# Performance work log

Measured on AMD Instinct MI355X. Metric: run time of the kernel, lower is better.

Reference implementation:

```python
import jax, jax.numpy as jnp
import numpy as np

B, V, T, CIN, WEMB, H, NW = 32, 500, 24, 2, 4, 64, 8
C0 = CIN + WEMB  # 6 channels entering first layer


def _stglstm(x, supports, Wg, bg, Wo, bo, out_len=None, final_layer=False):
    # x: (B, C, V, T); supports: (S, V, V)
    Bb, C, Vv, Tt = x.shape
    T_steps = out_len if out_len is not None else Tt
    if final_layer:
        xs = jnp.broadcast_to(x[:, :, :, -1][None], (T_steps, Bb, C, Vv))
    else:
        xs = jnp.moveaxis(x, 3, 0)  # (T, B, C, V)

    def step(carry, xt):
        hx, cx = carry
        comb = xt + hx  # (B, C, V)
        feats = [comb]
        for s in range(supports.shape[0]):  # fixed small support_len loop
            x1 = jnp.einsum('bcv,vw->bcw', comb, supports[s])
            x2 = jnp.einsum('bcv,vw->bcw', x1, supports[s])
            feats += [x1, x2]  # order-2 diffusion
        g = jnp.concatenate(feats, axis=1)  # (B, 7C, V)
        gates = jnp.einsum('bgv,og->bov', g, Wg) + bg[None, :, None]  # (B, 4C, V)
        i, f, cg, o = jnp.split(gates, 4, axis=1)
        cy = jax.nn.sigmoid(f) * cx + jax.nn.sigmoid(i) * cg  # cellgate is linear (no tanh), as in source
        hy = jax.nn.sigmoid(o) * jnp.tanh(cy)
        return (hy, cy), hy

    h0 = jnp.zeros((Bb, C, Vv), x.dtype)
    _, hs = jax.lax.scan(step, (h0, h0), xs)  # hs: (T, B, C, V)
    hs = jnp.moveaxis(hs, 0, 3)  # (B, C, V, T)
    return jnp.einsum('bcvt,oc->bovt', hs, Wo) + bo[None, :, None, None]


def _se(x, Wa, Wb):
    y = x.mean(axis=(2, 3))  # (B, C) global avg pool
    y = jax.nn.sigmoid(jax.nn.relu(y @ Wa.T) @ Wb.T)
    return x * y[:, :, None, None]


def setup_inputs():
    key = jax.random.key(0)
    ks = jax.random.split(key, 24)

    def n(k, shape, s=0.05):
        return jax.random.normal(k, shape, jnp.float32) * s

    A = jax.random.uniform(ks[0], (3, V, V), jnp.float32)
    A = A / A.sum(-1, keepdims=True)  # row-stochastic random-walk matrices
    return {
        'x': n(ks[1], (B, CIN, V, T), 1.0),
        'supports': A,
        'w_type': jax.random.randint(ks[2], (B, V, T), 0, NW, dtype=jnp.int32),
        'Wemb': n(ks[3], (NW, WEMB)),
        'Wg0': n(ks[4], (4 * C0, 7 * C0)), 'bg0': jnp.zeros((4 * C0,), jnp.float32),
        'Wo0': n(ks[5], (H, C0)), 'bo0': jnp.zeros((H,), jnp.float32),
        'Ws0a': n(ks[6], (H // 16, H)), 'Ws0b': n(ks[7], (H, H // 16)),
        'Wg1': n(ks[8], (4 * H, 7 * H)), 'bg1': jnp.zeros((4 * H,), jnp.float32),
        'Wo1': n(ks[9], (H, H)), 'bo1': jnp.zeros((H,), jnp.float32),
        'Ws1a': n(ks[10], (H // 16, H)), 'Ws1b': n(ks[11], (H, H // 16)),
        'Wg2': n(ks[12], (4 * H, 7 * H)), 'bg2': jnp.zeros((4 * H,), jnp.float32),
        'Wo2': n(ks[13], (H, H)), 'bo2': jnp.zeros((H,), jnp.float32),
        'Wg3': n(ks[14], (4 * H, 7 * H)), 'bg3': jnp.zeros((4 * H,), jnp.float32),
        'Wo3': n(ks[15], (2, H)), 'bo3': jnp.zeros((2,), jnp.float32),
    }


def reference(x, supports, w_type, Wemb, Wg0, bg0, Wo0, bo0, Ws0a, Ws0b,
              Wg1, bg1, Wo1, bo1, Ws1a, Ws1b, Wg2, bg2, Wo2, bo2,
              Wg3, bg3, Wo3, bo3):
    w_vec = Wemb[w_type]  # (B, V, T, wemb)
    w_vec = jnp.transpose(w_vec, (0, 3, 1, 2))  # (B, wemb, V, T)
    h = jnp.concatenate([x, w_vec], axis=1)  # (B, CIN+wemb, V, T)
    h = _stglstm(h, supports, Wg0, bg0, Wo0, bo0)
    h = _se(h, Ws0a, Ws0b)
    h = _stglstm(h, supports, Wg1, bg1, Wo1, bo1)
    h = _se(h, Ws1a, Ws1b)
    h = _stglstm(h, supports, Wg2, bg2, Wo2, bo2)
    out = _stglstm(h, supports, Wg3, bg3, Wo3, bo3, out_len=T, final_layer=True)
    return out  # (B, 2, V, out_len)
```

## Files before the change

### kernel.cpp

```cpp
#include <hip/hip_runtime.h>
#include <math.h>

#define NV 500
#define NB 32
#define NT 24
#define NH 64

typedef _Float16 f16;
typedef _Float16 f16x8 __attribute__((ext_vector_type(8)));
typedef _Float16 f16x4 __attribute__((ext_vector_type(4)));
typedef float    f32x4 __attribute__((ext_vector_type(4)));

__device__ __forceinline__ float sigm(float x){ return 1.f/(1.f+expf(-x)); }

__global__ void k_a2(const float* __restrict__ A, float* __restrict__ A2)
{
    int idx = blockIdx.x*256 + threadIdx.x;
    if (idx >= 3*500*500) return;
    int wv = idx % 500; int rest = idx/500; int r = rest % 500; int s = rest/500;
    const float* Ar = A + ((size_t)s*500 + r)*500;
    const float* Ac = A + (size_t)s*500*500 + wv;
    float a = 0.f;
    for (int u = 0; u < 500; u++) a += Ar[u]*Ac[(size_t)u*500];
    A2[idx] = a;
}

__global__ void k_acat(const float* __restrict__ A, const float* __restrict__ A2,
                       f16* __restrict__ AcatT)
{
    int idx = blockIdx.x*256 + threadIdx.x;
    if (idx >= 3072*512) return;
    int k = idx & 511;
    int n = idx >> 9;
    int j = n >> 9, wv = n & 511;
    float val = 0.f;
    if (k < 500 && wv < 500) {
        int s = j >> 1;
        const float* M = (j & 1) ? A2 : A;
        val = M[((size_t)s*500 + k)*500 + wv];
    }
    AcatT[idx] = (f16)val;
}

__global__ void k_f2h(const float* __restrict__ src, f16* __restrict__ dst, int n)
{
    int idx = blockIdx.x*256 + threadIdx.x;
    if (idx < n) dst[idx] = (f16)src[idx];
}

__global__ __launch_bounds__(256)
void k_diff(const f16* __restrict__ Acv, const f16* __restrict__ Bt,
            f16* __restrict__ fout, int Mtot, int C, int G)
{
    __shared__ f16 lA[128*32];
    __shared__ f16 lB[128*32];
    const int tid = threadIdx.x;
    const int n0 = blockIdx.x*128, m0 = blockIdx.y*128;
    const int r0 = tid>>2, c0 = tid&3;
    const int swz0 = r0*32 + ((c0 ^ ((r0>>1)&3))<<3);
    const int swz1 = swz0 + 64*32;
    int mA0 = m0 + r0;      if (mA0 > Mtot-1) mA0 = Mtot-1;
    int mA1 = m0 + r0 + 64; if (mA1 > Mtot-1) mA1 = Mtot-1;
    const f16* gA0 = Acv + (size_t)mA0*512 + c0*8;
    const f16* gA1 = Acv + (size_t)mA1*512 + c0*8;
    const f16* gB0 = Bt + (size_t)(n0+r0)*512 + c0*8;
    const f16* gB1 = Bt + (size_t)(n0+r0+64)*512 + c0*8;

    const int w = tid>>6, lane = tid&63;
    const int wr = (w>>1)<<6, wc = (w&1)<<6;
    const int fm = lane&15, fk = lane>>4;
    const int fch = (fk ^ ((fm>>1)&3))<<3;

    f32x4 acc[4][4];
    #pragma unroll
    for (int i=0;i<4;i++)
        #pragma unroll
        for (int j=0;j<4;j++) acc[i][j] = (f32x4){0.f,0.f,0.f,0.f};

    f32x4 ra0 = *(const f32x4*)gA0, ra1 = *(const f32x4*)gA1;
    f32x4 rb0 = *(const f32x4*)gB0, rb1 = *(const f32x4*)gB1;

    for (int ks = 0; ks < 16; ks++) {
        __syncthreads();
        *(f32x4*)(lA + swz0) = ra0;  *(f32x4*)(lA + swz1) = ra1;
        *(f32x4*)(lB + swz0) = rb0;  *(f32x4*)(lB + swz1) = rb1;
        if (ks < 15) {
            int o = (ks+1)*32;
            ra0 = *(const f32x4*)(gA0 + o); ra1 = *(const f32x4*)(gA1 + o);
            rb0 = *(const f32x4*)(gB0 + o); rb1 = *(const f32x4*)(gB1 + o);
        }
        __syncthreads();
        f16x8 af[4], bf[4];
        #pragma unroll
        for (int i=0;i<4;i++) af[i] = *(const f16x8*)(lA + (wr + i*16 + fm)*32 + fch);
        #pragma unroll
        for (int j=0;j<4;j++) bf[j] = *(const f16x8*)(lB + (wc + j*16 + fm)*32 + fch);
        #pragma unroll
        for (int i=0;i<4;i++)
            #pragma unroll
            for (int j=0;j<4;j++)
                acc[i][j] = __builtin_amdgcn_mfma_f32_16x16x32_f16(af[i], bf[j], acc[i][j], 0, 0, 0);
    }

    #pragma unroll
    for (int j=0;j<4;j++) {
        int col = n0 + wc + j*16 + fm;
        int jb = col >> 9, wv = col & 511;
        if (wv >= 500) continue;
        #pragma unroll
        for (int i=0;i<4;i++) {
            int mb = m0 + wr + i*16 + fk*4;
            if (C == 64) {
                if (mb >= Mtot) continue;
                int b = mb >> 6, c = mb & 63;
                f16x4 h4;
                h4[0]=(f16)acc[i][j][0]; h4[1]=(f16)acc[i][j][1];
                h4[2]=(f16)acc[i][j][2]; h4[3]=(f16)acc[i][j][3];
                *(f16x4*)(fout + ((size_t)b*512 + wv)*G + C + jb*C + c) = h4;
            } else {
                #pragma unroll
                for (int r=0;r<4;r++) {
                    int m = mb + r;
                    if (m < Mtot) {
                        int b = m / C, c = m - b*C;
                        fout[((size_t)b*512 + wv)*G + C + jb*C + c] = (f16)acc[i][j][r];
                    }
                }
            }
        }
    }
}

__global__ __launch_bounds__(256)
void k_gateslstm(const f16* __restrict__ fT, const f16* __restrict__ Wg,
                 const float* __restrict__ bg, float* __restrict__ cst,
                 const f16* __restrict__ Xn, f16* __restrict__ hsave,
                 const float* __restrict__ Wo3, const float* __restrict__ bo3,
                 float* __restrict__ out, int t,
                 f16* __restrict__ fTout, f16* __restrict__ ccv,
                 int first, int writecomb)
{
    __shared__ f16 lA[64*32];
    __shared__ f16 lB[256*32];
    __shared__ float ExF[4*64*65];
    __shared__ float bgS[256];
    __shared__ f16 combS[64*68];
    const int tid = threadIdx.x;
    const int m0 = blockIdx.x*64, b = blockIdx.y;
    const f16* Ab = fT + (size_t)b*512*448;
    bgS[tid] = bg[tid];

    const int r0 = tid>>2, c0 = tid&3;
    const int swz = r0*32 + ((c0 ^ ((r0>>1)&3))<<3);
    const f16* gA = Ab + (size_t)(m0+r0)*448 + c0*8;
    const f16* gB = Wg + (size_t)r0*448 + c0*8;

    const int w = tid>>6, lane = tid&63;
    const int wc = w<<6;
    const int fm = lane&15, fk = lane>>4;
    const int fch = (fk ^ ((fm>>1)&3))<<3;

    f32x4 acc[4][4];
    #pragma unroll
    for (int i=0;i<4;i++)
        #pragma unroll
        for (int j=0;j<4;j++) acc[i][j] = (f32x4){0.f,0.f,0.f,0.f};

    f32x4 ra  = *(const f32x4*)gA;
    f32x4 rb0 = *(const f32x4*)gB;
    f32x4 rb1 = *(const f32x4*)(gB + (size_t)64*448);
    f32x4 rb2 = *(const f32x4*)(gB + (size_t)128*448);
    f32x4 rb3 = *(const f32x4*)(gB + (size_t)192*448);

    for (int ks = 0; ks < 14; ks++) {
        __syncthreads();
        *(f32x4*)(lA + swz) = ra;
        *(f32x4*)(lB + swz)          = rb0;
        *(f32x4*)(lB + 64*32 + swz)  = rb1;
        *(f32x4*)(lB + 128*32 + swz) = rb2;
        *(f32x4*)(lB + 192*32 + swz) = rb3;
        if (ks < 13) {
            int o = (ks+1)*32;
            ra  = *(const f32x4*)(gA + o);
            rb0 = *(const f32x4*)(gB + o);
            rb1 = *(const f32x4*)(gB + (size_t)64*448 + o);
            rb2 = *(const f32x4*)(gB + (size_t)128*448 + o);
            rb3 = *(const f32x4*)(gB + (size_t)192*448 + o);
        }
        __syncthreads();
        f16x8 af[4], bf[4];
        #pragma unroll
        for (int i=0;i<4;i++) af[i] = *(const f16x8*)(lA + (i*16 + fm)*32 + fch);
        #pragma unroll
        for (int j=0;j<4;j++) bf[j] = *(const f16x8*)(lB + (wc + j*16 + fm)*32 + fch);
        #pragma unroll
        for (int i=0;i<4;i++)
            #pragma unroll
            for (int j=0;j<4;j++)
                acc[i][j] = __builtin_amdgcn_mfma_f32_16x16x32_f16(af[i], bf[j], acc[i][j], 0, 0, 0);
    }

    __syncthreads();
    #pragma unroll
    for (int i=0;i<4;i++)
        #pragma unroll
        for (int j=0;j<4;j++)
            #pragma unroll
            for (int r=0;r<4;r++)
                ExF[((w<<6) + i*16 + (fk<<2) + r)*65 + (j<<4) + fm] = acc[i][j][r];
    __syncthreads();

    const int vl = tid>>2, p = tid&3;
    const int v = m0 + vl;
    const size_t row = (size_t)b*512 + v;
    float hy[16];
    float* cp = cst + row*64 + (p<<4);
    #pragma unroll
    for (int k4=0;k4<4;k4++) {
        f32x4 cx4 = first ? (f32x4){0.f,0.f,0.f,0.f} : *(const f32x4*)(cp + k4*4);
        f32x4 cy4;
        #pragma unroll
        for (int e=0;e<4;e++) {
            int c = (p<<4) + k4*4 + e;
            float gi = ExF[(         vl)*65 + c] + bgS[c];
            float gf = ExF[( 64 +    vl)*65 + c] + bgS[64+c];
            float gc = ExF[(128 +    vl)*65 + c] + bgS[128+c];
            float go = ExF[(192 +    vl)*65 + c] + bgS[192+c];
            float cy = sigm(gf)*cx4[e] + sigm(gi)*gc;
            cy4[e] = cy;
            hy[k4*4+e] = sigm(go)*tanhf(cy);
        }
        *(f32x4*)(cp + k4*4) = cy4;
    }

    if (hsave) {
        alignas(16) f16 tmp[16];
        #pragma unroll
        for (int k=0;k<16;k++) tmp[k] = (f16)hy[k];
        f16* hp = hsave + row*64 + (p<<4);
        *(f32x4*)hp = *(f32x4*)tmp;
        *(f32x4*)(hp+8) = *(f32x4*)(tmp+8);
    }

    if (out) {
        float r0s = 0.f, r1s = 0.f;
        #pragma unroll
        for (int k=0;k<16;k++){ r0s += Wo3[(p<<4)+k]*hy[k]; r1s += Wo3[64+(p<<4)+k]*hy[k]; }
        r0s += __shfl_xor(r0s, 1, 64); r0s += __shfl_xor(r0s, 2, 64);
        r1s += __shfl_xor(r1s, 1, 64); r1s += __shfl_xor(r1s, 2, 64);
        if (p == 0 && v < 500) {
            out[((size_t)(b*2+0)*500 + v)*24 + t] = r0s + bo3[0];
            out[((size_t)(b*2+1)*500 + v)*24 + t] = r1s + bo3[1];
        }
    }

    if (writecomb) {
        alignas(16) f16 c16[16];
        if (v < 500) {
            const f16* xp = Xn + row*64 + (p<<4);
            alignas(16) f16 xv[16];
            *(f32x4*)xv = *(const f32x4*)xp;
            *(f32x4*)(xv+8) = *(const f32x4*)(xp+8);
            #pragma unroll
            for (int k=0;k<16;k++) c16[k] = (f16)((float)xv[k] + hy[k]);
        } else {
            #pragma unroll
            for (int k=0;k<16;k++) c16[k] = (f16)0.f;
        }
        f16* fp = fTout + row*448 + (p<<4);
        *(f32x4*)fp = *(f32x4*)c16;
        *(f32x4*)(fp+8) = *(f32x4*)(c16+8);
        #pragma unroll
        for (int k=0;k<16;k++) combS[vl*68 + (p<<4) + k] = c16[k];
        __syncthreads();
        const int c = tid>>2, jj = tid&3;
        alignas(16) f16 tmp[16];
        #pragma unroll
        for (int k=0;k<16;k++) tmp[k] = combS[(jj*16+k)*68 + c];
        f16* dst = ccv + ((size_t)b*64 + c)*512 + m0 + jj*16;
        *(f32x4*)dst = *(f32x4*)tmp;
        *(f32x4*)(dst+8) = *(f32x4*)(tmp+8);
    }
}

__global__ __launch_bounds__(256)
void k_seed(const f16* __restrict__ X0, f16* __restrict__ fT, f16* __restrict__ ccv)
{
    __shared__ f16 combS[64*68];
    const int b = blockIdx.y, v0 = blockIdx.x*64;
    const int tid = threadIdx.x, vl = tid>>2, p = tid&3;
    const int v = v0 + vl;
    const size_t row = (size_t)b*512 + v;
    alignas(16) f16 c16[16];
    if (v < 500) {
        const f16* xp = X0 + row*64 + p*16;
        *(f32x4*)c16 = *(const f32x4*)xp;
        *(f32x4*)(c16+8) = *(const f32x4*)(xp+8);
    } else {
        #pragma unroll
        for (int k=0;k<16;k++) c16[k] = (f16)0.f;
    }
    f16* fp = fT + row*448 + p*16;
    *(f32x4*)fp = *(f32x4*)c16;
    *(f32x4*)(fp+8) = *(f32x4*)(c16+8);
    #pragma unroll
    for (int k=0;k<16;k++) combS[vl*68 + p*16 + k] = c16[k];
    __syncthreads();
    const int c = tid>>2, j = tid&3;
    alignas(16) f16 tmp[16];
    #pragma unroll
    for (int k=0;k<16;k++) tmp[k] = combS[(j*16+k)*68 + c];
    f16* dst = ccv + ((size_t)b*64 + c)*512 + v0 + j*16;
    *(f32x4*)dst = *(f32x4*)tmp;
    *(f32x4*)(dst+8) = *(f32x4*)(tmp+8);
}

__global__ __launch_bounds__(256)
void k_xprojm(const f16* __restrict__ src, const f16* __restrict__ WoF,
              const float* __restrict__ bo, const float* __restrict__ se,
              f16* __restrict__ X)
{
    __shared__ f16 lA[128*64];
    __shared__ f16 lB[64*64];
    const int tid = threadIdx.x;
    const size_t m0 = (size_t)blockIdx.x*128;
    const int r0 = tid>>2, c0 = tid&3;
    const int swz = r0*32 + ((c0 ^ ((r0>>1)&3))<<3);
    const f16* gA0 = src + (m0 + r0)*64 + c0*8;
    const f16* gA1 = gA0 + 64*64;
    const f16* gB  = WoF + r0*64 + c0*8;

    *(f32x4*)(lA + swz)               = *(const f32x4*)gA0;
    *(f32x4*)(lA + 2048 + swz)        = *(const f32x4*)gA1;
    *(f32x4*)(lA + 4096 + swz)        = *(const f32x4*)(gA0 + 32);
    *(f32x4*)(lA + 6144 + swz)        = *(const f32x4*)(gA1 + 32);
    *(f32x4*)(lB + swz)               = *(const f32x4*)gB;
    *(f32x4*)(lB + 2048 + swz)        = *(const f32x4*)(gB + 32);
    __syncthreads();

    const int w = tid>>6, lane = tid&63;
    const int wr = w<<5;
    const int fm = lane&15, fk = lane>>4;
    const int fch = (fk ^ ((fm>>1)&3))<<3;

    f32x4 acc[2][4];
    #pragma unroll
    for (int i=0;i<2;i++)
        #pragma unroll
        for (int j=0;j<4;j++) acc[i][j] = (f32x4){0.f,0.f,0.f,0.f};

    #pragma unroll
    for (int ks=0; ks<2; ks++) {
        f16x8 af[2], bf[4];
        #pragma unroll
        for (int i=0;i<2;i++) af[i] = *(const f16x8*)(lA + ks*4096 + (wr + i*16 + fm)*32 + fch);
        #pragma unroll
        for (int j=0;j<4;j++) bf[j] = *(const f16x8*)(lB + ks*2048 + (j*16 + fm)*32 + fch);
        #pragma unroll
        for (int i=0;i<2;i++)
            #pragma unroll
            for (int j=0;j<4;j++)
                acc[i][j] = __builtin_amdgcn_mfma_f32_16x16x32_f16(af[i], bf[j], acc[i][j], 0, 0, 0);
    }
    __syncthreads();

    const int bb = (int)((m0 >> 9) & 31);
    #pragma unroll
    for (int j=0;j<4;j++) {
        const int c = (j<<4) + fm;
        const float bias = bo[c];
        const float sf = se ? se[bb*64 + c] : 1.f;
        #pragma unroll
        for (int i=0;i<2;i++) {
            const int rbase = wr + i*16 + (fk<<2);
            #pragma unroll
            for (int r=0;r<4;r++)
                lA[(rbase + r)*64 + c] = (f16)(sf*(acc[i][j][r] + bias));
        }
    }
    __syncthreads();
    #pragma unroll
    for (int pass=0; pass<4; pass++) {
        int chunk = pass*256 + tid;
        int row = chunk>>3, off = (chunk&7)<<3;
        *(f32x4*)(X + (m0 + row)*64 + off) = *(const f32x4*)(lA + row*64 + off);
    }
}

__global__ void k_xproj1(const float* __restrict__ src, const float* __restrict__ Wo,
                         const float* __restrict__ bo, const float* __restrict__ se,
                         f16* __restrict__ X, int total)
{
    int id = blockIdx.x*256 + threadIdx.x;
    if (id >= total) return;
    int c = id & 63;
    size_t row = (size_t)(id >> 6);
    int b = (int)((row >> 9) & 31);
    const float* sp = src + row*6;
    float a = bo[c];
    #pragma unroll
    for (int j=0;j<6;j++) a += Wo[c*6+j]*sp[j];
    X[id] = (f16)(se[b*64+c]*a);
}

__global__ void k_xe(const float* __restrict__ x, const int* __restrict__ wt,
                     const float* __restrict__ Wemb, float* __restrict__ XE)
{
    int id = blockIdx.x*256 + threadIdx.x;
    if (id >= NT*NB*512) return;
    int v = id & 511; int r = id >> 9; int b = r & 31; int t = r >> 5;
    float vals[6] = {0.f,0.f,0.f,0.f,0.f,0.f};
    if (v < 500) {
        vals[0] = x[((size_t)(b*2+0)*500 + v)*24 + t];
        vals[1] = x[((size_t)(b*2+1)*500 + v)*24 + t];
        int wty = wt[((size_t)b*500 + v)*24 + t];
        vals[2] = Wemb[wty*4+0]; vals[3] = Wemb[wty*4+1];
        vals[4] = Wemb[wty*4+2]; vals[5] = Wemb[wty*4+3];
    }
    float* xe = XE + (size_t)id*6;
    #pragma unroll
    for (int c = 0; c < 6; c++) xe[c] = vals[c];
}

__global__ void k_seed0(const float* __restrict__ XE, f16* __restrict__ f0T,
                        f16* __restrict__ ccv0)
{
    int id = blockIdx.x*256 + threadIdx.x;
    if (id >= NB*512) return;
    int v = id & 511, b = id >> 9;
    const float* xe = XE + (size_t)id*6;
    #pragma unroll
    for (int c = 0; c < 6; c++) {
        f16 h = (v < 500) ? (f16)xe[c] : (f16)0.f;
        f0T[(size_t)id*42 + c] = h;
        ccv0[((size_t)b*6 + c)*512 + v] = h;
    }
}

__global__ __launch_bounds__(256)
void k_glstm0(f16* f0T, const float* __restrict__ Wg0,
              const float* __restrict__ bg0, float* __restrict__ cst0,
              float* __restrict__ hs0T, const float* __restrict__ XE,
              f16* __restrict__ ccv0, int t)
{
    __shared__ float WgS[24*42];
    __shared__ float bgS[24];
    int tid = threadIdx.x;
    for (int i = tid; i < 24*42; i += 256) WgS[i] = Wg0[i];
    if (tid < 24) bgS[tid] = bg0[tid];
    __syncthreads();
    int id = blockIdx.x*256 + tid;
    if (id >= NB*500) return;
    int b = id / 500, v = id - b*500;
    const f16* fp = f0T + ((size_t)b*512 + v)*42;
    float fv[42];
    #pragma unroll
    for (int g = 0; g < 42; g++) fv[g] = (float)fp[g];
    float gates[24];
    #pragma unroll
    for (int o = 0; o < 24; o++) {
        float a = bgS[o];
        #pragma unroll
        for (int g = 0; g < 42; g++) a += WgS[o*42+g]*fv[g];
        gates[o] = a;
    }
    size_t hrow = (((size_t)t*NB + b)*512 + v)*6;
    const float* xe = XE + (((size_t)(t+1)*NB + b)*512 + v)*6;
    #pragma unroll
    for (int c = 0; c < 6; c++) {
        size_t ci = ((size_t)b*500 + v)*6 + c;
        float cx = t ? cst0[ci] : 0.f;
        float cy = sigm(gates[6+c])*cx + sigm(gates[c])*gates[12+c];
        cst0[ci] = cy;
        float h = sigm(gates[18+c])*tanhf(cy);
        hs0T[hrow + c] = h;
        if (t < 23) {
            float cmb = xe[c] + h;
            f0T[((size_t)b*512 + v)*42 + c] = (f16)cmb;
            ccv0[((size_t)b*6 + c)*512 + v] = (f16)cmb;
        }
    }
}

__global__ void k_mean0(const float* __restrict__ hs0T, float* __restrict__ mean0)
{
    int b = blockIdx.x;
    float acc[6] = {0,0,0,0,0,0};
    for (int i = threadIdx.x; i < 24*500; i += 256) {
        int tt = i/500, v = i - tt*500;
        const float* p = hs0T + (((size_t)tt*NB + b)*512 + v)*6;
        #pragma unroll
        for (int c=0;c<6;c++) acc[c] += p[c];
    }
    __shared__ float red[256];
    for (int c=0;c<6;c++) {
        red[threadIdx.x] = acc[c]; __syncthreads();
        for (int s=128;s>0;s>>=1) { if (threadIdx.x<s) red[threadIdx.x]+=red[threadIdx.x+s]; __syncthreads(); }
        if (threadIdx.x==0) mean0[b*6+c] = red[0]/12000.f;
        __syncthreads();
    }
}

__global__ void k_mean1(const f16* __restrict__ hs1T, float* __restrict__ mean1)
{
    int cg = blockIdx.x, b = blockIdx.y;
    float acc[8] = {0,0,0,0,0,0,0,0};
    for (int i = threadIdx.x; i < 24*500; i += 256) {
        int tt = i/500, v = i - tt*500;
        const f16* p = hs1T + (((size_t)tt*NB + b)*512 + v)*64 + cg*8;
        #pragma unroll
        for (int c=0;c<8;c++) acc[c] += (float)p[c];
    }
    __shared__ float red[256];
    for (int c=0;c<8;c++) {
        red[threadIdx.x] = acc[c]; __syncthreads();
        for (int s=128;s>0;s>>=1) { if (threadIdx.x<s) red[threadIdx.x]+=red[threadIdx.x+s]; __syncthreads(); }
        if (threadIdx.x==0) mean1[b*64 + cg*8 + c] = red[0]/12000.f;
        __syncthreads();
    }
}

__global__ void k_se(const float* __restrict__ meanhs, const float* __restrict__ Wo,
                     const float* __restrict__ bo, int Cin,
                     const float* __restrict__ Wa, const float* __restrict__ Wb,
                     float* __restrict__ se)
{
    int b = blockIdx.x; int c = threadIdx.x;
    __shared__ float y[64]; __shared__ float a[4];
    float acc = bo[c];
    for (int j = 0; j < Cin; j++) acc += Wo[(size_t)c*Cin + j] * meanhs[b*Cin + j];
    y[c] = acc;
    __syncthreads();
    if (c < 4) {
        float s = 0.f;
        for (int j = 0; j < 64; j++) s += Wa[c*64 + j] * y[j];
        a[c] = fmaxf(s, 0.f);
    }
    __syncthreads();
    float s = 0.f;
    #pragma unroll
    for (int j = 0; j < 4; j++) s += Wb[c*4 + j] * a[j];
    se[b*64 + c] = 1.f/(1.f + expf(-s));
}

extern "C" void kernel_launch(void* const* d_in, const int* in_sizes, int n_in,
                              void* d_out, int out_size, void* d_ws, size_t ws_size,
                              hipStream_t stream)
{
    const float* x    = (const float*)d_in[0];
    const float* sup  = (const float*)d_in[1];
    const int*   wt   = (const int*)  d_in[2];
    const float* Wemb = (const float*)d_in[3];
    const float* Wg0  = (const float*)d_in[4];
    const float* bg0  = (const float*)d_in[5];
    const float* Wo0  = (const float*)d_in[6];
    const float* bo0  = (const float*)d_in[7];
    const float* Wa0  = (const float*)d_in[8];
    const float* Wb0  = (const float*)d_in[9];
    const float* Wg1  = (const float*)d_in[10];
    const float* bg1  = (const float*)d_in[11];
    const float* Wo1  = (const float*)d_in[12];
    const float* bo1  = (const float*)d_in[13];
    const float* Wa1  = (const float*)d_in[14];
    const float* Wb1  = (const float*)d_in[15];
    const float* Wg2  = (const float*)d_in[16];
    const float* bg2  = (const float*)d_in[17];
    const float* Wo2  = (const float*)d_in[18];
    const float* bo2  = (const float*)d_in[19];
    const float* Wg3  = (const float*)d_in[20];
    const float* bg3  = (const float*)d_in[21];
    const float* Wo3  = (const float*)d_in[22];
    const float* bo3  = (const float*)d_in[23];
    float* out = (float*)d_out;
    (void)in_sizes; (void)n_in; (void)out_size; (void)ws_size;

    char* ws = (char*)d_ws;
    size_t off = 0;
    f16*   AcatT  = (f16*)(ws + off);   off += (size_t)3072*512*2;
    float* A2     = (float*)(ws + off); off += (size_t)3*500*500*4;
    f16*   WgF1   = (f16*)(ws + off);   off += (size_t)256*448*2;
    f16*   WgF2   = (f16*)(ws + off);   off += (size_t)256*448*2;
    f16*   WgF3   = (f16*)(ws + off);   off += (size_t)256*448*2;
    f16*   WoF1   = (f16*)(ws + off);   off += (size_t)64*64*2;
    f16*   WoF2   = (f16*)(ws + off);   off += (size_t)64*64*2;
    f16*   comb_cv= (f16*)(ws + off);   off += (size_t)2048*512*2;
    f16*   ccv0   = (f16*)(ws + off);   off += (size_t)192*512*2;
    f16*   featsT = (f16*)(ws + off);   off += (size_t)NB*512*448*2;
    f16*   f0T    = (f16*)(ws + off);   off += (size_t)NB*512*42*2;
    float* XE     = (float*)(ws + off); off += (size_t)NT*NB*512*6*4;
    float* hs0T   = (float*)(ws + off); off += (size_t)NT*NB*512*6*4;
    f16*   hs1T   = (f16*)(ws + off);   off += (size_t)NT*NB*512*64*2;
    f16*   hT     = (f16*)(ws + off);   off += (size_t)NB*512*64*2;
    float* cstT   = (float*)(ws + off); off += (size_t)NB*512*64*4;
    float* cst0   = (float*)(ws + off); off += (size_t)NB*500*6*4;
    f16*   Xbuf   = (f16*)(ws + off);   off += (size_t)NT*NB*512*64*2;
    f16*   X3     = (f16*)(ws + off);   off += (size_t)NB*512*64*2;
    float* mean0  = (float*)(ws + off); off += 8192;
    float* se0    = (float*)(ws + off); off += 8192;
    float* mean1  = (float*)(ws + off); off += 8192;
    float* se1    = (float*)(ws + off); off += 8192;

    const size_t sliceH = (size_t)NB*512*64;

    k_a2  <<<(3*500*500 + 255)/256, 256, 0, stream>>>(sup, A2);
    k_acat<<<(3072*512 + 255)/256, 256, 0, stream>>>(sup, A2, AcatT);
    k_f2h <<<(256*448 + 255)/256, 256, 0, stream>>>(Wg1, WgF1, 256*448);
    k_f2h <<<(256*448 + 255)/256, 256, 0, stream>>>(Wg2, WgF2, 256*448);
    k_f2h <<<(256*448 + 255)/256, 256, 0, stream>>>(Wg3, WgF3, 256*448);
    k_f2h <<<16, 256, 0, stream>>>(Wo1, WoF1, 64*64);
    k_f2h <<<16, 256, 0, stream>>>(Wo2, WoF2, 64*64);
    k_xe  <<<(NT*NB*512)/256, 256, 0, stream>>>(x, wt, Wemb, XE);

    k_seed0<<<(NB*512)/256, 256, 0, stream>>>(XE, f0T, ccv0);
    for (int t = 0; t < NT; t++) {
        k_diff  <<<dim3(24, 2), 256, 0, stream>>>(ccv0, AcatT, f0T, 192, 6, 42);
        k_glstm0<<<(NB*500 + 255)/256, 256, 0, stream>>>(f0T, Wg0, bg0, cst0, hs0T, XE, ccv0, t);
    }
    k_mean0<<<NB, 256, 0, stream>>>(hs0T, mean0);
    k_se   <<<NB, 64, 0, stream>>>(mean0, Wo0, bo0, 6, Wa0, Wb0, se0);

    k_xproj1<<<(NT*NB*512*64)/256, 256, 0, stream>>>(hs0T, Wo0, bo0, se0, Xbuf, NT*NB*512*64);
    k_seed <<<dim3(8, NB), 256, 0, stream>>>(Xbuf, featsT, comb_cv);
    for (int t = 0; t < NT; t++) {
        k_diff <<<dim3(24, 16), 256, 0, stream>>>(comb_cv, AcatT, featsT, 2048, 64, 448);
        k_gateslstm<<<dim3(8, NB), 256, 0, stream>>>(featsT, WgF1, bg1, cstT,
                 (t < 23) ? Xbuf + (size_t)(t+1)*sliceH : (const f16*)nullptr,
                 hs1T + (size_t)t*sliceH, nullptr, nullptr, nullptr, t,
                 featsT, comb_cv, t == 0, t < 23);
    }
    k_mean1<<<dim3(8, NB), 256, 0, stream>>>(hs1T, mean1);
    k_se   <<<NB, 64, 0, stream>>>(mean1, Wo1, bo1, 64, Wa1, Wb1, se1);

    k_xprojm<<<(NT*NB*512)/128, 256, 0, stream>>>(hs1T, WoF1, bo1, se1, Xbuf);
    k_seed <<<dim3(8, NB), 256, 0, stream>>>(Xbuf, featsT, comb_cv);
    for (int t = 0; t < NT; t++) {
        k_diff <<<dim3(24, 16), 256, 0, stream>>>(comb_cv, AcatT, featsT, 2048, 64, 448);
        k_gateslstm<<<dim3(8, NB), 256, 0, stream>>>(featsT, WgF2, bg2, cstT,
                 (t < 23) ? Xbuf + (size_t)(t+1)*sliceH : (const f16*)nullptr,
                 (t == 23) ? hT : (f16*)nullptr, nullptr, nullptr, nullptr, t,
                 featsT, comb_cv, t == 0, t < 23);
    }

    k_xprojm<<<(NB*512)/128, 256, 0, stream>>>(hT, WoF2, bo2, nullptr, X3);
    k_seed <<<dim3(8, NB), 256, 0, stream>>>(X3, featsT, comb_cv);
    for (int t = 0; t < NT; t++) {
        k_diff <<<dim3(24, 16), 256, 0, stream>>>(comb_cv, AcatT, featsT, 2048, 64, 448);
        k_gateslstm<<<dim3(8, NB), 256, 0, stream>>>(featsT, WgF3, bg3, cstT,
                 X3, nullptr, Wo3, bo3, out, t,
                 featsT, comb_cv, t == 0, t < 23);
    }
}
```

Measured before the change: 4.593 ms.

## Split gates GEMM from LSTM update and compute A² with MFMA GEMM

```diff
diff --git a/kernel.cpp b/kernel.cpp
--- a/kernel.cpp
+++ b/kernel.cpp
@@ -13,33 +13,95 @@
 
 __device__ __forceinline__ float sigm(float x){ return 1.f/(1.f+expf(-x)); }
 
-__global__ void k_a2(const float* __restrict__ A, float* __restrict__ A2)
-{
-    int idx = blockIdx.x*256 + threadIdx.x;
-    if (idx >= 3*500*500) return;
-    int wv = idx % 500; int rest = idx/500; int r = rest % 500; int s = rest/500;
-    const float* Ar = A + ((size_t)s*500 + r)*500;
-    const float* Ac = A + (size_t)s*500*500 + wv;
-    float a = 0.f;
-    for (int u = 0; u < 500; u++) a += Ar[u]*Ac[(size_t)u*500];
-    A2[idx] = a;
-}
-
-__global__ void k_acat(const float* __restrict__ A, const float* __restrict__ A2,
-                       f16* __restrict__ AcatT)
-{
-    int idx = blockIdx.x*256 + threadIdx.x;
-    if (idx >= 3072*512) return;
-    int k = idx & 511;
-    int n = idx >> 9;
-    int j = n >> 9, wv = n & 511;
-    float val = 0.f;
-    if (k < 500 && wv < 500) {
-        int s = j >> 1;
-        const float* M = (j & 1) ? A2 : A;
-        val = M[((size_t)s*500 + k)*500 + wv];
-    }
-    AcatT[idx] = (f16)val;
+__global__ __launch_bounds__(256)
+void k_prep_a(const float* __restrict__ A, f16* __restrict__ AcatT, f16* __restrict__ A16)
+{
+    __shared__ float t[64][65];
+    const int s = blockIdx.z;
+    const int v0 = blockIdx.y*64, w0 = blockIdx.x*64;
+    const float* As = A + (size_t)s*500*500;
+    const int tid = threadIdx.x;
+    for (int e = tid; e < 64*64; e += 256) {
+        int r = e>>6, c = e&63;
+        int v = v0+r, w = w0+c;
+        float val = (v < 500 && w < 500) ? As[(size_t)v*500 + w] : 0.f;
+        t[r][c] = val;
+        A16[((size_t)s*512 + v)*512 + w] = (f16)val;
+    }
+    __syncthreads();
+    for (int e = tid; e < 64*64; e += 256) {
+        int wr = e>>6, vc = e&63;
+        AcatT[((size_t)(2*s)*512 + w0+wr)*512 + v0+vc] = (f16)t[vc][wr];
+    }
+}
+
+__global__ __launch_bounds__(256)
+void k_a2m(f16* __restrict__ AcatT, const f16* __restrict__ A16)
+{
+    __shared__ f16 lA[128*32];
+    __shared__ f16 lB[128*32];
+    const int tid = threadIdx.x;
+    const int s = blockIdx.z;
+    const int n0 = blockIdx.x*128, m0 = blockIdx.y*128;
+    const f16* AT = AcatT + (size_t)(2*s)*512*512;
+    const f16* Y  = A16 + (size_t)s*512*512;
+    f16* D = AcatT + (size_t)(2*s+1)*512*512;
+
+    const int r0 = tid>>2, c0 = tid&3;
+    const int swz0 = r0*32 + ((c0 ^ ((r0>>1)&3))<<3);
+    const int swz1 = swz0 + 64*32;
+    const f16* gA0 = AT + (size_t)(m0+r0)*512 + c0*8;
+    const f16* gA1 = AT + (size_t)(m0+r0+64)*512 + c0*8;
+    const f16* gB0 = Y + (size_t)(n0+r0)*512 + c0*8;
+    const f16* gB1 = Y + (size_t)(n0+r0+64)*512 + c0*8;
+
+    const int w = tid>>6, lane = tid&63;
+    const int wr = (w>>1)<<6, wc = (w&1)<<6;
+    const int fm = lane&15, fk = lane>>4;
+    const int fch = (fk ^ ((fm>>1)&3))<<3;
+
+    f32x4 acc[4][4];
+    #pragma unroll
+    for (int i=0;i<4;i++)
+        #pragma unroll
+        for (int j=0;j<4;j++) acc[i][j] = (f32x4){0.f,0.f,0.f,0.f};
+
+    f32x4 ra0 = *(const f32x4*)gA0, ra1 = *(const f32x4*)gA1;
+    f32x4 rb0 = *(const f32x4*)gB0, rb1 = *(const f32x4*)gB1;
+
+    for (int ks = 0; ks < 16; ks++) {
+        __syncthreads();
+        *(f32x4*)(lA + swz0) = ra0;  *(f32x4*)(lA + swz1) = ra1;
+        *(f32x4*)(lB + swz0) = rb0;  *(f32x4*)(lB + swz1) = rb1;
+        if (ks < 15) {
+            int o = (ks+1)*32;
+            ra0 = *(const f32x4*)(gA0 + o); ra1 = *(const f32x4*)(gA1 + o);
+            rb0 = *(const f32x4*)(gB0 + o); rb1 = *(const f32x4*)(gB1 + o);
+        }
+        __syncthreads();
+        f16x8 af[4], bf[4];
+        #pragma unroll
+        for (int i=0;i<4;i++) af[i] = *(const f16x8*)(lA + (wr + i*16 + fm)*32 + fch);
+        #pragma unroll
+        for (int j=0;j<4;j++) bf[j] = *(const f16x8*)(lB + (wc + j*16 + fm)*32 + fch);
+        #pragma unroll
+        for (int i=0;i<4;i++)
+            #pragma unroll
+            for (int j=0;j<4;j++)
+                acc[i][j] = __builtin_amdgcn_mfma_f32_16x16x32_f16(af[i], bf[j], acc[i][j], 0, 0, 0);
+    }
+
+    #pragma unroll
+    for (int j=0;j<4;j++) {
+        int col = n0 + wc + j*16 + fm;
+        #pragma unroll
+        for (int i=0;i<4;i++) {
+            int mb = m0 + wr + i*16 + fk*4;
+            #pragma unroll
+            for (int r=0;r<4;r++)
+                D[(size_t)(mb+r)*512 + col] = (f16)acc[i][j][r];
+        }
+    }
 }
 
 __global__ void k_f2h(const float* __restrict__ src, f16* __restrict__ dst, int n)
@@ -132,31 +194,24 @@
 }
 
 __global__ __launch_bounds__(256)
-void k_gateslstm(const f16* __restrict__ fT, const f16* __restrict__ Wg,
-                 const float* __restrict__ bg, float* __restrict__ cst,
-                 const f16* __restrict__ Xn, f16* __restrict__ hsave,
-                 const float* __restrict__ Wo3, const float* __restrict__ bo3,
-                 float* __restrict__ out, int t,
-                 f16* __restrict__ fTout, f16* __restrict__ ccv,
-                 int first, int writecomb)
-{
-    __shared__ f16 lA[64*32];
-    __shared__ f16 lB[256*32];
-    __shared__ float ExF[4*64*65];
-    __shared__ float bgS[256];
-    __shared__ f16 combS[64*68];
+void k_gates(const f16* __restrict__ fT, const f16* __restrict__ Wg,
+             const float* __restrict__ bg, f16* __restrict__ gT)
+{
+    __shared__ f16 lA[128*32];
+    __shared__ f16 lB[128*32];
     const int tid = threadIdx.x;
-    const int m0 = blockIdx.x*64, b = blockIdx.y;
+    const int n0 = blockIdx.x*128, m0 = blockIdx.y*128, b = blockIdx.z;
     const f16* Ab = fT + (size_t)b*512*448;
-    bgS[tid] = bg[tid];
-
     const int r0 = tid>>2, c0 = tid&3;
-    const int swz = r0*32 + ((c0 ^ ((r0>>1)&3))<<3);
-    const f16* gA = Ab + (size_t)(m0+r0)*448 + c0*8;
-    const f16* gB = Wg + (size_t)r0*448 + c0*8;
+    const int swz0 = r0*32 + ((c0 ^ ((r0>>1)&3))<<3);
+    const int swz1 = swz0 + 64*32;
+    const f16* gA0 = Ab + (size_t)(m0+r0)*448 + c0*8;
+    const f16* gA1 = Ab + (size_t)(m0+r0+64)*448 + c0*8;
+    const f16* gB0 = Wg + (size_t)(n0+r0)*448 + c0*8;
+    const f16* gB1 = Wg + (size_t)(n0+r0+64)*448 + c0*8;
 
     const int w = tid>>6, lane = tid&63;
-    const int wc = w<<6;
+    const int wr = (w>>1)<<6, wc = (w&1)<<6;
     const int fm = lane&15, fk = lane>>4;
     const int fch = (fk ^ ((fm>>1)&3))<<3;
 
@@ -166,31 +221,22 @@
         #pragma unroll
         for (int j=0;j<4;j++) acc[i][j] = (f32x4){0.f,0.f,0.f,0.f};
 
-    f32x4 ra  = *(const f32x4*)gA;
-    f32x4 rb0 = *(const f32x4*)gB;
-    f32x4 rb1 = *(const f32x4*)(gB + (size_t)64*448);
-    f32x4 rb2 = *(const f32x4*)(gB + (size_t)128*448);
-    f32x4 rb3 = *(const f32x4*)(gB + (size_t)192*448);
+    f32x4 ra0 = *(const f32x4*)gA0, ra1 = *(const f32x4*)gA1;
+    f32x4 rb0 = *(const f32x4*)gB0, rb1 = *(const f32x4*)gB1;
 
     for (int ks = 0; ks < 14; ks++) {
         __syncthreads();
-        *(f32x4*)(lA + swz) = ra;
-        *(f32x4*)(lB + swz)          = rb0;
-        *(f32x4*)(lB + 64*32 + swz)  = rb1;
-        *(f32x4*)(lB + 128*32 + swz) = rb2;
-        *(f32x4*)(lB + 192*32 + swz) = rb3;
+        *(f32x4*)(lA + swz0) = ra0;  *(f32x4*)(lA + swz1) = ra1;
+        *(f32x4*)(lB + swz0) = rb0;  *(f32x4*)(lB + swz1) = rb1;
         if (ks < 13) {
             int o = (ks+1)*32;
-            ra  = *(const f32x4*)(gA + o);
-            rb0 = *(const f32x4*)(gB + o);
-            rb1 = *(const f32x4*)(gB + (size_t)64*448 + o);
-            rb2 = *(const f32x4*)(gB + (size_t)128*448 + o);
-            rb3 = *(const f32x4*)(gB + (size_t)192*448 + o);
+            ra0 = *(const f32x4*)(gA0 + o); ra1 = *(const f32x4*)(gA1 + o);
+            rb0 = *(const f32x4*)(gB0 + o); rb1 = *(const f32x4*)(gB1 + o);
         }
         __syncthreads();
         f16x8 af[4], bf[4];
         #pragma unroll
-        for (int i=0;i<4;i++) af[i] = *(const f16x8*)(lA + (i*16 + fm)*32 + fch);
+        for (int i=0;i<4;i++) af[i] = *(const f16x8*)(lA + (wr + i*16 + fm)*32 + fch);
         #pragma unroll
         for (int j=0;j<4;j++) bf[j] = *(const f16x8*)(lB + (wc + j*16 + fm)*32 + fch);
         #pragma unroll
@@ -200,35 +246,58 @@
                 acc[i][j] = __builtin_amdgcn_mfma_f32_16x16x32_f16(af[i], bf[j], acc[i][j], 0, 0, 0);
     }
 
-    __syncthreads();
-    #pragma unroll
-    for (int i=0;i<4;i++)
-        #pragma unroll
-        for (int j=0;j<4;j++)
-            #pragma unroll
-            for (int r=0;r<4;r++)
-                ExF[((w<<6) + i*16 + (fk<<2) + r)*65 + (j<<4) + fm] = acc[i][j][r];
-    __syncthreads();
-
-    const int vl = tid>>2, p = tid&3;
-    const int v = m0 + vl;
+    #pragma unroll
+    for (int j=0;j<4;j++) {
+        int o = n0 + wc + j*16 + fm;
+        float bias = bg[o];
+        #pragma unroll
+        for (int i=0;i<4;i++) {
+            int vb = m0 + wr + i*16 + fk*4;
+            #pragma unroll
+            for (int r=0;r<4;r++) {
+                int v = vb + r;
+                if (v < 500)
+                    gT[((size_t)b*512 + v)*256 + o] = (f16)(acc[i][j][r] + bias);
+            }
+        }
+    }
+}
+
+__global__ __launch_bounds__(256)
+void k_lstmcomb(const f16* __restrict__ gT, float* __restrict__ cst,
+                const f16* __restrict__ Xn, f16* __restrict__ hsave,
+                const float* __restrict__ Wo3, const float* __restrict__ bo3,
+                float* __restrict__ out, int t,
+                f16* __restrict__ fT, f16* __restrict__ ccv,
+                int first, int writecomb)
+{
+    __shared__ f16 combS[64*68];
+    const int b = blockIdx.y, v0 = blockIdx.x*64;
+    const int tid = threadIdx.x, vl = tid>>2, p = tid&3;
+    const int v = v0 + vl;
     const size_t row = (size_t)b*512 + v;
+    const f16* g = gT + row*256 + (p<<4);
+    alignas(16) f16 gq[4][16];
+    #pragma unroll
+    for (int q = 0; q < 4; q++) {
+        *(f32x4*)&gq[q][0] = *(const f32x4*)(g + q*64);
+        *(f32x4*)&gq[q][8] = *(const f32x4*)(g + q*64 + 8);
+    }
+
+    float* cp = cst + row*64 + (p<<4);
     float hy[16];
-    float* cp = cst + row*64 + (p<<4);
-    #pragma unroll
-    for (int k4=0;k4<4;k4++) {
+    #pragma unroll
+    for (int k4 = 0; k4 < 4; k4++) {
         f32x4 cx4 = first ? (f32x4){0.f,0.f,0.f,0.f} : *(const f32x4*)(cp + k4*4);
         f32x4 cy4;
         #pragma unroll
-        for (int e=0;e<4;e++) {
-            int c = (p<<4) + k4*4 + e;
-            float gi = ExF[(         vl)*65 + c] + bgS[c];
-            float gf = ExF[( 64 +    vl)*65 + c] + bgS[64+c];
-            float gc = ExF[(128 +    vl)*65 + c] + bgS[128+c];
-            float go = ExF[(192 +    vl)*65 + c] + bgS[192+c];
+        for (int e = 0; e < 4; e++) {
+            int kk = k4*4+e;
+            float gi = (float)gq[0][kk], gf = (float)gq[1][kk];
+            float gc = (float)gq[2][kk], go = (float)gq[3][kk];
             float cy = sigm(gf)*cx4[e] + sigm(gi)*gc;
             cy4[e] = cy;
-            hy[k4*4+e] = sigm(go)*tanhf(cy);
+            hy[kk] = sigm(go)*tanhf(cy);
         }
         *(f32x4*)(cp + k4*4) = cy4;
     }
@@ -243,14 +312,14 @@
     }
 
     if (out) {
-        float r0s = 0.f, r1s = 0.f;
-        #pragma unroll
-        for (int k=0;k<16;k++){ r0s += Wo3[(p<<4)+k]*hy[k]; r1s += Wo3[64+(p<<4)+k]*hy[k]; }
-        r0s += __shfl_xor(r0s, 1, 64); r0s += __shfl_xor(r0s, 2, 64);
-        r1s += __shfl_xor(r1s, 1, 64); r1s += __shfl_xor(r1s, 2, 64);
+        float r0 = 0.f, r1 = 0.f;
+        #pragma unroll
+        for (int k=0;k<16;k++){ r0 += Wo3[(p<<4)+k]*hy[k]; r1 += Wo3[64+(p<<4)+k]*hy[k]; }
+        r0 += __shfl_xor(r0, 1, 64); r0 += __shfl_xor(r0, 2, 64);
+        r1 += __shfl_xor(r1, 1, 64); r1 += __shfl_xor(r1, 2, 64);
         if (p == 0 && v < 500) {
-            out[((size_t)(b*2+0)*500 + v)*24 + t] = r0s + bo3[0];
-            out[((size_t)(b*2+1)*500 + v)*24 + t] = r1s + bo3[1];
+            out[((size_t)(b*2+0)*500 + v)*24 + t] = r0 + bo3[0];
+            out[((size_t)(b*2+1)*500 + v)*24 + t] = r1 + bo3[1];
         }
     }
 
@@ -267,7 +336,7 @@
             #pragma unroll
             for (int k=0;k<16;k++) c16[k] = (f16)0.f;
         }
-        f16* fp = fTout + row*448 + (p<<4);
+        f16* fp = fT + row*448 + (p<<4);
         *(f32x4*)fp = *(f32x4*)c16;
         *(f32x4*)(fp+8) = *(f32x4*)(c16+8);
         #pragma unroll
@@ -277,7 +346,7 @@
         alignas(16) f16 tmp[16];
         #pragma unroll
         for (int k=0;k<16;k++) tmp[k] = combS[(jj*16+k)*68 + c];
-        f16* dst = ccv + ((size_t)b*64 + c)*512 + m0 + jj*16;
+        f16* dst = ccv + ((size_t)b*64 + c)*512 + v0 + jj*16;
         *(f32x4*)dst = *(f32x4*)tmp;
         *(f32x4*)(dst+8) = *(f32x4*)(tmp+8);
     }
@@ -577,7 +646,7 @@
     char* ws = (char*)d_ws;
     size_t off = 0;
     f16*   AcatT  = (f16*)(ws + off);   off += (size_t)3072*512*2;
-    float* A2     = (float*)(ws + off); off += (size_t)3*500*500*4;
+    f16*   A16    = (f16*)(ws + off);   off += (size_t)3*512*512*2;
     f16*   WgF1   = (f16*)(ws + off);   off += (size_t)256*448*2;
     f16*   WgF2   = (f16*)(ws + off);   off += (size_t)256*448*2;
     f16*   WgF3   = (f16*)(ws + off);   off += (size_t)256*448*2;
@@ -587,6 +656,7 @@
     f16*   ccv0   = (f16*)(ws + off);   off += (size_t)192*512*2;
     f16*   featsT = (f16*)(ws + off);   off += (size_t)NB*512*448*2;
     f16*   f0T    = (f16*)(ws + off);   off += (size_t)NB*512*42*2;
+    f16*   gatesT = (f16*)(ws + off);   off += (size_t)NB*512*256*2;
     float* XE     = (float*)(ws + off); off += (size_t)NT*NB*512*6*4;
     float* hs0T   = (float*)(ws + off); off += (size_t)NT*NB*512*6*4;
     f16*   hs1T   = (f16*)(ws + off);   off += (size_t)NT*NB*512*64*2;
@@ -601,9 +671,11 @@
     float* se1    = (float*)(ws + off); off += 8192;
 
     const size_t sliceH = (size_t)NB*512*64;
-
-    k_a2  <<<(3*500*500 + 255)/256, 256, 0, stream>>>(sup, A2);
-    k_acat<<<(3072*512 + 255)/256, 256, 0, stream>>>(sup, A2, AcatT);
+    const size_t slice0 = 0;
+    (void)slice0;
+
+    k_prep_a<<<dim3(8, 8, 3), 256, 0, stream>>>(sup, AcatT, A16);
+    k_a2m   <<<dim3(4, 4, 3), 256, 0, stream>>>(AcatT, A16);
     k_f2h <<<(256*448 + 255)/256, 256, 0, stream>>>(Wg1, WgF1, 256*448);
     k_f2h <<<(256*448 + 255)/256, 256, 0, stream>>>(Wg2, WgF2, 256*448);
     k_f2h <<<(256*448 + 255)/256, 256, 0, stream>>>(Wg3, WgF3, 256*448);
@@ -623,7 +695,8 @@
     k_seed <<<dim3(8, NB), 256, 0, stream>>>(Xbuf, featsT, comb_cv);
     for (int t = 0; t < NT; t++) {
         k_diff <<<dim3(24, 16), 256, 0, stream>>>(comb_cv, AcatT, featsT, 2048, 64, 448);
-        k_gateslstm<<<dim3(8, NB), 256, 0, stream>>>(featsT, WgF1, bg1, cstT,
+        k_gates<<<dim3(2, 4, NB), 256, 0, stream>>>(featsT, WgF1, bg1, gatesT);
+        k_lstmcomb<<<dim3(8, NB), 256, 0, stream>>>(gatesT, cstT,
                  (t < 23) ? Xbuf + (size_t)(t+1)*sliceH : (const f16*)nullptr,
                  hs1T + (size_t)t*sliceH, nullptr, nullptr, nullptr, t,
                  featsT, comb_cv, t == 0, t < 23);
@@ -635,7 +708,8 @@
     k_seed <<<dim3(8, NB), 256, 0, stream>>>(Xbuf, featsT, comb_cv);
     for (int t = 0; t < NT; t++) {
         k_diff <<<dim3(24, 16), 256, 0, stream>>>(comb_cv, AcatT, featsT, 2048, 64, 448);
-        k_gateslstm<<<dim3(8, NB), 256, 0, stream>>>(featsT, WgF2, bg2, cstT,
+        k_gates<<<dim3(2, 4, NB), 256, 0, stream>>>(featsT, WgF2, bg2, gatesT);
+        k_lstmcomb<<<dim3(8, NB), 256, 0, stream>>>(gatesT, cstT,
                  (t < 23) ? Xbuf + (size_t)(t+1)*sliceH : (const f16*)nullptr,
                  (t == 23) ? hT : (f16*)nullptr, nullptr, nullptr, nullptr, t,
                  featsT, comb_cv, t == 0, t < 23);
@@ -645,8 +719,9 @@
     k_seed <<<dim3(8, NB), 256, 0, stream>>>(X3, featsT, comb_cv);
     for (int t = 0; t < NT; t++) {
         k_diff <<<dim3(24, 16), 256, 0, stream>>>(comb_cv, AcatT, featsT, 2048, 64, 448);
-        k_gateslstm<<<dim3(8, NB), 256, 0, stream>>>(featsT, WgF3, bg3, cstT,
-                 X3, nullptr, Wo3, bo3, out, t,
+        k_gates<<<dim3(2, 4, NB), 256, 0, stream>>>(featsT, WgF3, bg3, gatesT);
+        k_lstmcomb<<<dim3(8, NB), 256, 0, stream>>>(gatesT, cstT, X3,
+                 nullptr, Wo3, bo3, out, t,
                  featsT, comb_cv, t == 0, t < 23);
     }
 }
```

Measured after the change: 5.196 ms. 13.1% more time.
